# Kernel tuning notes

Hardware: AMD Instinct MI355X
Metric: run time of the kernel (lower is better)

The kernel has to match this reference:

```python
import jax, jax.numpy as jnp
import numpy as np

B = 1_048_576
NUM_USERS = 6041
NUM_MOVIES = 3953
EMB_DIM = 32
NUM_GENRES = 18
HIDDEN = [64, 32, 16]
WIDE_DIM = NUM_USERS + NUM_MOVIES + 3 + NUM_GENRES  # gender, age, occupation scalars
DEEP_IN = 2 * EMB_DIM + 3 + NUM_GENRES              # = 85


def setup_inputs() -> dict:
    key = jax.random.key(0)
    ks = jax.random.split(key, 20)
    inp = {
        "user_ids": jax.random.randint(ks[0], (B,), 0, NUM_USERS),
        "movie_ids": jax.random.randint(ks[1], (B,), 0, NUM_MOVIES),
        "gender": jax.random.uniform(ks[2], (B,), dtype=jnp.float32),
        "age": jax.random.uniform(ks[3], (B,), dtype=jnp.float32),
        "occupation": jax.random.uniform(ks[4], (B,), dtype=jnp.float32),
        "genres": jax.random.uniform(ks[5], (B, NUM_GENRES), dtype=jnp.float32),
        # wide linear (out_features=1): weight vector + scalar bias
        "wide_W": jax.random.normal(ks[6], (WIDE_DIM,), dtype=jnp.float32) * 0.01,
        "wide_b": jnp.zeros((), dtype=jnp.float32),
        # embedding tables
        "user_table": jax.random.normal(ks[7], (NUM_USERS, EMB_DIM), dtype=jnp.float32) * 0.05,
        "movie_table": jax.random.normal(ks[8], (NUM_MOVIES, EMB_DIM), dtype=jnp.float32) * 0.05,
        # deep MLP params (stored as [in, out])
        "W1": jax.random.normal(ks[9], (DEEP_IN, HIDDEN[0]), dtype=jnp.float32) * 0.05,
        "b1": jnp.zeros((HIDDEN[0],), dtype=jnp.float32),
        "W2": jax.random.normal(ks[10], (HIDDEN[0], HIDDEN[1]), dtype=jnp.float32) * 0.05,
        "b2": jnp.zeros((HIDDEN[1],), dtype=jnp.float32),
        "W3": jax.random.normal(ks[11], (HIDDEN[1], HIDDEN[2]), dtype=jnp.float32) * 0.05,
        "b3": jnp.zeros((HIDDEN[2],), dtype=jnp.float32),
        "W4": jax.random.normal(ks[12], (HIDDEN[2], 1), dtype=jnp.float32) * 0.05,
        "b4": jnp.zeros((1,), dtype=jnp.float32),
    }
    return inp


def reference(user_ids, movie_ids, gender, age, occupation, genres,
              wide_W, wide_b, user_table, movie_table,
              W1, b1, W2, b2, W3, b3, W4, b4):
    nu = user_table.shape[0]
    nm = movie_table.shape[0]
    # dense (non-one-hot) part of the wide input: [B, 3 + num_genres]
    rest = jnp.concatenate(
        [gender[:, None], age[:, None], occupation[:, None], genres], axis=1)
    # one_hot @ W  ==  gather of the corresponding weight entries (same math,
    # without materializing the [B, nu+nm+21] one-hot matrix)
    w_user = wide_W[:nu]
    w_movie = wide_W[nu:nu + nm]
    w_rest = wide_W[nu + nm:]
    wide_out = w_user[user_ids] + w_movie[movie_ids] + rest @ w_rest + wide_b  # [B]

    # deep path (dropout is identity at inference)
    u_emb = user_table[user_ids]    # [B, 32]
    m_emb = movie_table[movie_ids]  # [B, 32]
    h = jnp.concatenate([u_emb, m_emb, rest], axis=1)  # [B, 85]
    h = jax.nn.relu(h @ W1 + b1)
    h = jax.nn.relu(h @ W2 + b2)
    h = jax.nn.relu(h @ W3 + b3)
    deep_out = (h @ W4 + b4)[:, 0]  # [B]

    return jax.nn.sigmoid(wide_out + deep_out)  # [B]
```

## Files before the change

kernel.cpp:

```cpp
#include <hip/hip_runtime.h>

#define NUSERS  6041
#define NMOVIES 3953
#define EMB     32
#define NGEN    18
#define H1N     64
#define H2N     32
#define H3N     16

typedef __bf16 bf16_t;
typedef bf16_t bf16x8 __attribute__((ext_vector_type(8)));
typedef bf16_t bf16x4 __attribute__((ext_vector_type(4)));
typedef float  f32x4  __attribute__((ext_vector_type(4)));
typedef float  f32x8  __attribute__((ext_vector_type(8)));

__device__ __forceinline__ f32x4 mfma16(bf16x8 a, bf16x8 b, f32x4 c) {
    return __builtin_amdgcn_mfma_f32_16x16x32_bf16(a, b, c, 0, 0, 0);
}
__device__ __forceinline__ bf16x8 cvt8(f32x8 v) {
    bf16x8 o;
    #pragma unroll
    for (int i = 0; i < 8; ++i) o[i] = (bf16_t)v[i];
    return o;
}

#define L1STRIDE 68
#define L2STRIDE 36
#define RSTRIDE  28
#define RBUFSZ   (16 * RSTRIDE)

#define RESTW 24
#define PREPROWS 512

#define TAB_U4   (NUSERS * EMB / 4)
#define TAB_M4   (NMOVIES * EMB / 4)
#define TAB4TOT  (TAB_U4 + TAB_M4)

__device__ __forceinline__ void pack_rest_row(const float* __restrict__ x,
                                              float gg, float aa, float oo,
                                              bf16_t* __restrict__ op)
{
    bf16x8 c0, c1, c2;
    c0[0] = (bf16_t)gg;   c0[1] = (bf16_t)aa;   c0[2] = (bf16_t)oo;
    c0[3] = (bf16_t)x[0]; c0[4] = (bf16_t)x[1]; c0[5] = (bf16_t)x[2];
    c0[6] = (bf16_t)x[3]; c0[7] = (bf16_t)x[4];
    #pragma unroll
    for (int j = 0; j < 8; ++j) c1[j] = (bf16_t)x[5 + j];
    #pragma unroll
    for (int j = 0; j < 5; ++j) c2[j] = (bf16_t)x[13 + j];
    c2[5] = (bf16_t)0.0f;
    c2[6] = (bf16_t)1.0f;
    c2[7] = (bf16_t)0.0f;
    *(bf16x8*)(op)      = c0;
    *(bf16x8*)(op + 8)  = c1;
    *(bf16x8*)(op + 16) = c2;
}

__global__ __launch_bounds__(256)
void prep_all(const float* __restrict__ gender,
              const float* __restrict__ age,
              const float* __restrict__ occupation,
              const float* __restrict__ genres,
              const float* __restrict__ user_table,
              const float* __restrict__ movie_table,
              bf16_t* __restrict__ rest,
              bf16_t* __restrict__ utab,
              bf16_t* __restrict__ mtab,
              int n)
{
    const int t  = threadIdx.x;
    const int b  = blockIdx.x;
    const int gB = (n + PREPROWS - 1) / PREPROWS;

    if (b < gB) {
        const int r0 = b * PREPROWS;
        if ((n & 1) == 0) {
            __shared__ float gbuf[PREPROWS * NGEN];
            const float4* gsrc = (const float4*)genres;
            const int totF4  = (n * NGEN) >> 2;
            const int f4base = (r0 >> 1) * 9;
            #pragma unroll
            for (int s = 0; s < 9; ++s) {
                const int gi = t + s * 256;
                int idx = f4base + gi;
                if (idx > totF4 - 1) idx = totF4 - 1;
                *(float4*)(gbuf + gi * 4) = gsrc[idx];
            }
            __syncthreads();
            #pragma unroll
            for (int rr = 0; rr < 2; ++rr) {
                const int lr = t + rr * 256;
                const int r  = r0 + lr;
                if (r < n) {
                    float x[NGEN];
                    #pragma unroll
                    for (int c = 0; c < NGEN; ++c) x[c] = gbuf[lr * NGEN + c];
                    pack_rest_row(x, gender[r], age[r], occupation[r],
                                  rest + (size_t)r * RESTW);
                }
            }
        } else {
            for (int rr = 0; rr < 2; ++rr) {
                const int r = r0 + t + rr * 256;
                if (r < n) {
                    const float* gr = genres + (size_t)r * NGEN;
                    float x[NGEN];
                    #pragma unroll
                    for (int c = 0; c < NGEN; ++c) x[c] = gr[c];
                    pack_rest_row(x, gender[r], age[r], occupation[r],
                                  rest + (size_t)r * RESTW);
                }
            }
        }
    } else {
        const int u = (b - gB) * 256 + t;
        if (u < TAB4TOT) {
            if (u < TAB_U4) {
                float4 v = *(const float4*)(user_table + (size_t)u * 4);
                bf16x4 o; o[0]=(bf16_t)v.x; o[1]=(bf16_t)v.y; o[2]=(bf16_t)v.z; o[3]=(bf16_t)v.w;
                *(bf16x4*)(utab + (size_t)u * 4) = o;
            } else {
                const int w = u - TAB_U4;
                float4 v = *(const float4*)(movie_table + (size_t)w * 4);
                bf16x4 o; o[0]=(bf16_t)v.x; o[1]=(bf16_t)v.y; o[2]=(bf16_t)v.z; o[3]=(bf16_t)v.w;
                *(bf16x4*)(mtab + (size_t)w * 4) = o;
            }
        }
    }
}

__global__ __launch_bounds__(256, 2)
void wd_fwd_main(const int*   __restrict__ user_ids,
                 const int*   __restrict__ movie_ids,
                 const float* __restrict__ wide_W,
                 const float* __restrict__ wide_b,
                 const float* __restrict__ W1,
                 const float* __restrict__ b1,
                 const float* __restrict__ W2,
                 const float* __restrict__ b2,
                 const float* __restrict__ W3,
                 const float* __restrict__ b3,
                 const float* __restrict__ W4,
                 const float* __restrict__ b4,
                 const bf16_t* __restrict__ utab,
                 const bf16_t* __restrict__ mtab,
                 const bf16_t* __restrict__ rest,
                 float*       __restrict__ out,
                 int n)
{
    const int lane = threadIdx.x & 63;
    const int m    = lane & 15;
    const int quad = lane >> 4;

    bf16x8 B1f[3][4];
    #pragma unroll
    for (int kt = 0; kt < 3; ++kt)
        #pragma unroll
        for (int nt = 0; nt < 4; ++nt) {
            bf16x8 f;
            #pragma unroll
            for (int j = 0; j < 8; ++j) {
                const int k = kt * 32 + quad * 8 + j;
                float v;
                if (k < 85)       v = W1[k * H1N + nt * 16 + m];
                else if (k == 86) v = b1[nt * 16 + m];
                else              v = 0.0f;
                f[j] = (bf16_t)v;
            }
            B1f[kt][nt] = f;
        }
    bf16x8 Bwf;
    {
        const float* wr = wide_W + NUSERS + NMOVIES;
        #pragma unroll
        for (int j = 0; j < 8; ++j) {
            const int k = 64 + quad * 8 + j;
            float v = 0.0f;
            if (m == 0) { if (k < 85) v = wr[k - 64]; else if (k == 85) v = 1.0f; }
            Bwf[j] = (bf16_t)v;
        }
    }
    bf16x8 B2f[2][2];
    #pragma unroll
    for (int kt = 0; kt < 2; ++kt)
        #pragma unroll
        for (int nt = 0; nt < 2; ++nt) {
            bf16x8 f;
            #pragma unroll
            for (int j = 0; j < 8; ++j) {
                const int u = (2 * kt + (j >> 2)) * 16 + quad * 4 + (j & 3);
                f[j] = (bf16_t)W2[u * H2N + nt * 16 + m];
            }
            B2f[kt][nt] = f;
        }
    bf16x8 B3f;
    #pragma unroll
    for (int j = 0; j < 8; ++j) {
        const int u = (j >> 2) * 16 + quad * 4 + (j & 3);
        B3f[j] = (bf16_t)W3[u * H3N + m];
    }

    f32x4 bias2[2], bias3, w4f;
    bias2[0] = *(const f32x4*)(b2 + quad * 4);
    bias2[1] = *(const f32x4*)(b2 + 16 + quad * 4);
    bias3    = *(const f32x4*)(b3 + quad * 4);
    w4f      = *(const f32x4*)(W4 + quad * 4);
    const float b4v = b4[0];
    const float wb0 = wide_b[0];

    const int ntiles = (n + 15) >> 4;
    const int gwave  = (blockIdx.x * blockDim.x + threadIdx.x) >> 6;
    const int nwaves = (gridDim.x * blockDim.x) >> 6;
    int niter = 0;
    if (gwave < ntiles) niter = (ntiles - gwave + nwaves - 1) / nwaves;
    if (niter == 0) return;

    int t_c = gwave;
    int t_n = t_c + nwaves; if (t_n >= ntiles) t_n = t_c;

    int rc = t_c * 16 + m; if (rc >= n) rc = n - 1;
    int uid_c = user_ids[rc], mid_c = movie_ids[rc];
    bf16x8 A0c = *(const bf16x8*)(utab + (size_t)uid_c * EMB + quad * 8);
    bf16x8 A1c = *(const bf16x8*)(mtab + (size_t)mid_c * EMB + quad * 8);
    bf16x8 A2c;
    #pragma unroll
    for (int j = 0; j < 8; ++j) A2c[j] = (bf16_t)0.0f;
    if (quad < 3) A2c = *(const bf16x8*)(rest + (size_t)rc * RESTW + quad * 8);
    float wuc = 0.0f, wmc = 0.0f;
    if (quad == 2) { wuc = wide_W[uid_c]; wmc = wide_W[NUSERS + mid_c]; }
    int rn = t_n * 16 + m; if (rn >= n) rn = n - 1;
    int uid_n = user_ids[rn], mid_n = movie_ids[rn];

    for (int i = 0; i < niter; ++i) {
        const bool more = (i + 1 < niter);
        bf16x8 A0n = A0c, A1n = A1c, A2n;
        #pragma unroll
        for (int j = 0; j < 8; ++j) A2n[j] = (bf16_t)0.0f;
        float wun = wuc, wmn = wmc;
        int uid_n2 = uid_n, mid_n2 = mid_n;
        int t_n2 = t_n;
        if (more) {
            A0n = *(const bf16x8*)(utab + (size_t)uid_n * EMB + quad * 8);
            A1n = *(const bf16x8*)(mtab + (size_t)mid_n * EMB + quad * 8);
            int rx = t_n * 16 + m; if (rx >= n) rx = n - 1;
            if (quad < 3) A2n = *(const bf16x8*)(rest + (size_t)rx * RESTW + quad * 8);
            wun = 0.0f; wmn = 0.0f;
            if (quad == 2) { wun = wide_W[uid_n]; wmn = wide_W[NUSERS + mid_n]; }
            t_n2 = t_n + nwaves; if (t_n2 >= ntiles) t_n2 = t_n;
            int r2 = t_n2 * 16 + m; if (r2 >= n) r2 = n - 1;
            uid_n2 = user_ids[r2]; mid_n2 = movie_ids[r2];
        }

        bf16x8 A2 = A2c;
        if (quad == 2) A2[5] = (bf16_t)(wuc + wmc + wb0);

        f32x4 accw = mfma16(Bwf, A2, (f32x4){0.f, 0.f, 0.f, 0.f});

        f32x4 acc[4];
        #pragma unroll
        for (int nt = 0; nt < 4; ++nt) {
            f32x4 c = {0.f, 0.f, 0.f, 0.f};
            c = mfma16(B1f[2][nt], A2,  c);
            c = mfma16(B1f[1][nt], A1c, c);
            c = mfma16(B1f[0][nt], A0c, c);
            acc[nt] = c;
        }

        bf16x8 AL2[2];
        #pragma unroll
        for (int kt = 0; kt < 2; ++kt) {
            bf16x8 f;
            #pragma unroll
            for (int r = 0; r < 4; ++r) {
                f[r]     = (bf16_t)fmaxf(acc[2 * kt][r],     0.0f);
                f[4 + r] = (bf16_t)fmaxf(acc[2 * kt + 1][r], 0.0f);
            }
            AL2[kt] = f;
        }

        f32x4 acc2[2];
        #pragma unroll
        for (int nt = 0; nt < 2; ++nt) {
            f32x4 c = bias2[nt];
            c = mfma16(B2f[0][nt], AL2[0], c);
            c = mfma16(B2f[1][nt], AL2[1], c);
            acc2[nt] = c;
        }

        bf16x8 AL3;
        #pragma unroll
        for (int r = 0; r < 4; ++r) {
            AL3[r]     = (bf16_t)fmaxf(acc2[0][r], 0.0f);
            AL3[4 + r] = (bf16_t)fmaxf(acc2[1][r], 0.0f);
        }

        f32x4 acc3 = mfma16(B3f, AL3, bias3);

        float p = fmaxf(acc3[0], 0.0f) * w4f[0]
                + fmaxf(acc3[1], 0.0f) * w4f[1]
                + fmaxf(acc3[2], 0.0f) * w4f[2]
                + fmaxf(acc3[3], 0.0f) * w4f[3];
        p += __shfl_xor(p, 16, 64);
        p += __shfl_xor(p, 32, 64);
        if (lane < 16) {
            const int orow = (t_c << 4) + lane;
            if (orow < n) {
                const float zv = p + accw[0] + b4v;
                out[orow] = 1.0f / (1.0f + __expf(-zv));
            }
        }

        if (more) {
            A0c = A0n; A1c = A1n; A2c = A2n;
            wuc = wun; wmc = wmn;
            uid_n = uid_n2; mid_n = mid_n2;
            t_c = t_n; t_n = t_n2;
        }
    }
}

struct Pref {
    float4 u0, u1, m0, m1;
    float  wu, wm;
};

__global__ __launch_bounds__(256)
void wd_fwd_pipe(const int*   __restrict__ user_ids,
                 const int*   __restrict__ movie_ids,
                 const float* __restrict__ gender,
                 const float* __restrict__ age,
                 const float* __restrict__ occupation,
                 const float* __restrict__ genres,
                 const float* __restrict__ wide_W,
                 const float* __restrict__ wide_b,
                 const float* __restrict__ user_table,
                 const float* __restrict__ movie_table,
                 const float* __restrict__ W1,
                 const float* __restrict__ b1,
                 const float* __restrict__ W2,
                 const float* __restrict__ b2,
                 const float* __restrict__ W3,
                 const float* __restrict__ b3,
                 const float* __restrict__ W4,
                 const float* __restrict__ b4,
                 float*       __restrict__ out,
                 int n)
{
    const int lane = threadIdx.x & 63;
    const int wib  = threadIdx.x >> 6;
    const int m    = lane & 15;
    const int quad = lane >> 4;

    __shared__ float lds_rest[4][2 * RBUFSZ];
    __shared__ float lds1[4][16 * L1STRIDE];
    __shared__ float lds2[4][16 * L2STRIDE];
    float* __restrict__ rbase = lds_rest[wib];
    float* __restrict__ L1p   = lds1[wib];
    float* __restrict__ L2p   = lds2[wib];

    for (int k = lane; k < 2 * RBUFSZ; k += 64) rbase[k] = 0.0f;

    bf16x8 B1f[3][4];
    #pragma unroll
    for (int kt = 0; kt < 3; ++kt)
        #pragma unroll
        for (int nt = 0; nt < 4; ++nt) {
            bf16x8 f;
            #pragma unroll
            for (int j = 0; j < 8; ++j) {
                const int k  = kt * 32 + quad * 8 + j;
                const float v = (k < 85) ? W1[k * H1N + nt * 16 + m] : 0.0f;
                f[j] = (bf16_t)v;
            }
            B1f[kt][nt] = f;
        }
    bf16x8 Bwf;
    {
        const float* wr = wide_W + NUSERS + NMOVIES;
        #pragma unroll
        for (int j = 0; j < 8; ++j) {
            const int k = 64 + quad * 8 + j;
            float v = 0.0f;
            if (m == 0) { if (k < 85) v = wr[k - 64]; else if (k == 85) v = 1.0f; }
            Bwf[j] = (bf16_t)v;
        }
    }
    bf16x8 B2f[2][2];
    #pragma unroll
    for (int kt = 0; kt < 2; ++kt)
        #pragma unroll
        for (int nt = 0; nt < 2; ++nt) {
            bf16x8 f;
            #pragma unroll
            for (int j = 0; j < 8; ++j)
                f[j] = (bf16_t)W2[(kt * 32 + quad * 8 + j) * H2N + nt * 16 + m];
            B2f[kt][nt] = f;
        }
    bf16x8 B3f;
    #pragma unroll
    for (int j = 0; j < 8; ++j) B3f[j] = (bf16_t)W3[(quad * 8 + j) * H3N + m];

    float bias1[4], bias2[2];
    #pragma unroll
    for (int nt = 0; nt < 4; ++nt) bias1[nt] = b1[nt * 16 + m];
    #pragma unroll
    for (int nt = 0; nt < 2; ++nt) bias2[nt] = b2[nt * 16 + m];
    const float bias3 = b3[m];
    const float w4v   = W4[m];
    const float b4v   = b4[0];
    const float wb0   = wide_b[0];

    const int ntiles = (n + 15) >> 4;
    const int gwave  = blockIdx.x * 4 + wib;
    const int nwaves = gridDim.x * 4;
    int niter = 0;
    if (gwave < ntiles) niter = (ntiles - gwave + nwaves - 1) / nwaves;
    const long gmax = (long)n * NGEN - 1;

#define LOAD_IDS(tt, U, M) { int rr = (tt) * 16 + m; rr = rr < n ? rr : n - 1; \
                             U = user_ids[rr]; M = movie_ids[rr]; }
#define LOAD_GENRES(tt, G, SC) { \
    const long gb = (long)(tt) * (16 * NGEN); \
    _Pragma("unroll") \
    for (int r = 0; r < 4; ++r) { long idx = gb + lane + r * 64; \
        idx = idx < gmax ? idx : gmax; G[r] = genres[idx]; } \
    { long idx = gb + lane + 256; idx = idx < gmax ? idx : gmax; \
      G[4] = (lane < 32) ? genres[idx] : 0.0f; } \
    { int rr = (tt) * 16 + m; rr = rr < n ? rr : n - 1; \
      const float* sp = (quad == 0) ? gender : (quad == 1) ? age : occupation; \
      SC = (quad < 3) ? sp[rr] : 0.0f; } }
#define WRITE_RBUF(B, G, SC) { \
    float* rb_ = rbase + (B) * RBUFSZ; \
    _Pragma("unroll") \
    for (int r = 0; r < 4; ++r) { int gi = lane + r * 64; int rw = gi / NGEN; \
        int cl = gi - rw * NGEN; rb_[rw * RSTRIDE + 3 + cl] = G[r]; } \
    if (lane < 32) { int gi = lane + 256; int rw = gi / NGEN; int cl = gi - rw * NGEN; \
        rb_[rw * RSTRIDE + 3 + cl] = G[4]; } \
    if (quad < 3) rb_[m * RSTRIDE + quad] = SC; }
#define ISSUE_GATHER(UID, MID, P) { \
    const float4* up_ = (const float4*)(user_table + (size_t)(UID) * EMB + quad * 8); \
    P.u0 = up_[0]; P.u1 = up_[1]; \
    const float4* mp_ = (const float4*)(movie_table + (size_t)(MID) * EMB + quad * 8); \
    P.m0 = mp_[0]; P.m1 = mp_[1]; \
    P.wu = wide_W[UID]; P.wm = wide_W[NUSERS + (MID)]; }

    if (niter > 0) {
        int t_c = gwave;
        int t_n = t_c + nwaves; if (t_n >= ntiles) t_n = t_c;

        int uid_c, mid_c, uid_n, mid_n, uid_n2, mid_n2;
        float gg_c[5], sc_c, gg_n[5], sc_n;
        Pref P_c, P_n;

        LOAD_IDS(t_c, uid_c, mid_c);
        LOAD_GENRES(t_c, gg_c, sc_c);
        ISSUE_GATHER(uid_c, mid_c, P_c);
        LOAD_IDS(t_n, uid_n, mid_n);
        WRITE_RBUF(0, gg_c, sc_c);
        uid_n2 = uid_n; mid_n2 = mid_n;
        int buf = 0;

        for (int i = 0; i < niter; ++i) {
            const float* rb = rbase + buf * RBUFSZ;
            const float4* sA = (const float4*)(rb + m * RSTRIDE + quad * 8);
            float4 a2a = sA[0], a2b = sA[1];

            const bool more = (i + 1 < niter);
            int t_n2 = t_n;
            if (more) {
                LOAD_GENRES(t_n, gg_n, sc_n);
                ISSUE_GATHER(uid_n, mid_n, P_n);
                t_n2 = t_n + nwaves; if (t_n2 >= ntiles) t_n2 = t_n;
                LOAD_IDS(t_n2, uid_n2, mid_n2);
            }

            const int base = t_c << 4;
            f32x8 vf;
            vf[0]=P_c.u0.x; vf[1]=P_c.u0.y; vf[2]=P_c.u0.z; vf[3]=P_c.u0.w;
            vf[4]=P_c.u1.x; vf[5]=P_c.u1.y; vf[6]=P_c.u1.z; vf[7]=P_c.u1.w;
            bf16x8 A0 = cvt8(vf);
            vf[0]=P_c.m0.x; vf[1]=P_c.m0.y; vf[2]=P_c.m0.z; vf[3]=P_c.m0.w;
            vf[4]=P_c.m1.x; vf[5]=P_c.m1.y; vf[6]=P_c.m1.z; vf[7]=P_c.m1.w;
            bf16x8 A1 = cvt8(vf);
            vf[0]=a2a.x; vf[1]=a2a.y; vf[2]=a2a.z; vf[3]=a2a.w;
            vf[4]=a2b.x; vf[5]=a2b.y; vf[6]=a2b.z; vf[7]=a2b.w;
            if (quad == 2) vf[5] = P_c.wu + P_c.wm + wb0;
            bf16x8 A2 = cvt8(vf);

            f32x4 accw = mfma16(A2, Bwf, (f32x4){0.f, 0.f, 0.f, 0.f});

            f32x4 acc[4];
            #pragma unroll
            for (int nt = 0; nt < 4; ++nt) {
                f32x4 c = {bias1[nt], bias1[nt], bias1[nt], bias1[nt]};
                c = mfma16(A0, B1f[0][nt], c);
                c = mfma16(A1, B1f[1][nt], c);
                c = mfma16(A2, B1f[2][nt], c);
                acc[nt] = c;
            }
            #pragma unroll
            for (int nt = 0; nt < 4; ++nt)
                #pragma unroll
                for (int r = 0; r < 4; ++r)
                    L1p[(quad * 4 + r) * L1STRIDE + nt * 16 + m] = fmaxf(acc[nt][r], 0.0f);

            bf16x8 AL2[2];
            #pragma unroll
            for (int kt = 0; kt < 2; ++kt) {
                const float4* s = (const float4*)(L1p + m * L1STRIDE + kt * 32 + quad * 8);
                float4 a = s[0], b = s[1];
                f32x8 t8; t8[0]=a.x; t8[1]=a.y; t8[2]=a.z; t8[3]=a.w;
                t8[4]=b.x; t8[5]=b.y; t8[6]=b.z; t8[7]=b.w;
                AL2[kt] = cvt8(t8);
            }

            f32x4 acc2[2];
            #pragma unroll
            for (int nt = 0; nt < 2; ++nt) {
                f32x4 c = {bias2[nt], bias2[nt], bias2[nt], bias2[nt]};
                c = mfma16(AL2[0], B2f[0][nt], c);
                c = mfma16(AL2[1], B2f[1][nt], c);
                acc2[nt] = c;
            }
            #pragma unroll
            for (int nt = 0; nt < 2; ++nt)
                #pragma unroll
                for (int r = 0; r < 4; ++r)
                    L2p[(quad * 4 + r) * L2STRIDE + nt * 16 + m] = fmaxf(acc2[nt][r], 0.0f);

            bf16x8 AL3;
            {
                const float4* s = (const float4*)(L2p + m * L2STRIDE + quad * 8);
                float4 a = s[0], b = s[1];
                f32x8 t8; t8[0]=a.x; t8[1]=a.y; t8[2]=a.z; t8[3]=a.w;
                t8[4]=b.x; t8[5]=b.y; t8[6]=b.z; t8[7]=b.w;
                AL3 = cvt8(t8);
            }

            f32x4 acc3 = mfma16(AL3, B3f, (f32x4){bias3, bias3, bias3, bias3});

            float t0 = fmaxf(acc3[0], 0.0f) * w4v + accw[0];
            float t1 = fmaxf(acc3[1], 0.0f) * w4v + accw[1];
            float t2 = fmaxf(acc3[2], 0.0f) * w4v + accw[2];
            float t3 = fmaxf(acc3[3], 0.0f) * w4v + accw[3];
            #pragma unroll
            for (int off = 1; off < 16; off <<= 1) {
                t0 += __shfl_xor(t0, off, 64);
                t1 += __shfl_xor(t1, off, 64);
                t2 += __shfl_xor(t2, off, 64);
                t3 += __shfl_xor(t3, off, 64);
            }
            if (m < 4) {
                float zv = t0;
                zv = (m == 1) ? t1 : zv;
                zv = (m == 2) ? t2 : zv;
                zv = (m == 3) ? t3 : zv;
                zv += b4v;
                const int orow = base + quad * 4 + m;
                if (orow < n) out[orow] = 1.0f / (1.0f + __expf(-zv));
            }

            if (more) {
                WRITE_RBUF(buf ^ 1, gg_n, sc_n);
                P_c = P_n;
                uid_c = uid_n; mid_c = mid_n;
                uid_n = uid_n2; mid_n = mid_n2;
                t_c = t_n; t_n = t_n2;
                buf ^= 1;
            }
        }
    }
#undef LOAD_IDS
#undef LOAD_GENRES
#undef WRITE_RBUF
#undef ISSUE_GATHER
}

extern "C" void kernel_launch(void* const* d_in, const int* in_sizes, int n_in,
                              void* d_out, int out_size, void* d_ws, size_t ws_size,
                              hipStream_t stream)
{
    const int*   user_ids   = (const int*)  d_in[0];
    const int*   movie_ids  = (const int*)  d_in[1];
    const float* gender     = (const float*)d_in[2];
    const float* age        = (const float*)d_in[3];
    const float* occupation = (const float*)d_in[4];
    const float* genres     = (const float*)d_in[5];
    const float* wide_W     = (const float*)d_in[6];
    const float* wide_b     = (const float*)d_in[7];
    const float* user_table = (const float*)d_in[8];
    const float* movie_table= (const float*)d_in[9];
    const float* W1         = (const float*)d_in[10];
    const float* b1         = (const float*)d_in[11];
    const float* W2         = (const float*)d_in[12];
    const float* b2         = (const float*)d_in[13];
    const float* W3         = (const float*)d_in[14];
    const float* b3         = (const float*)d_in[15];
    const float* W4         = (const float*)d_in[16];
    const float* b4         = (const float*)d_in[17];
    float*       out        = (float*)d_out;

    const int n = in_sizes[0];

    const size_t utab_bytes = ((size_t)NUSERS  * EMB * 2 + 255) & ~(size_t)255;
    const size_t mtab_bytes = ((size_t)NMOVIES * EMB * 2 + 255) & ~(size_t)255;
    const size_t rest_bytes = (size_t)n * RESTW * 2;
    const size_t need = utab_bytes + mtab_bytes + rest_bytes;

    if (d_ws != nullptr && ws_size >= need) {
        bf16_t* utab = (bf16_t*)d_ws;
        bf16_t* mtab = (bf16_t*)((char*)d_ws + utab_bytes);
        bf16_t* rest = (bf16_t*)((char*)d_ws + utab_bytes + mtab_bytes);

        const int gB      = (n + PREPROWS - 1) / PREPROWS;
        const int tblocks = (TAB4TOT + 255) / 256;
        prep_all<<<gB + tblocks, 256, 0, stream>>>(gender, age, occupation, genres,
                                                   user_table, movie_table,
                                                   rest, utab, mtab, n);
        wd_fwd_main<<<1024, 256, 0, stream>>>(user_ids, movie_ids, wide_W, wide_b,
                                              W1, b1, W2, b2, W3, b3, W4, b4,
                                              utab, mtab, rest, out, n);
    } else {
        wd_fwd_pipe<<<1024, 256, 0, stream>>>(user_ids, movie_ids, gender, age, occupation,
                                              genres, wide_W, wide_b, user_table, movie_table,
                                              W1, b1, W2, b2, W3, b3, W4, b4, out, n);
    }
}
```

Baseline: 217.5 us.

## Prepack MLP weight fragments in prep kernel and launch single-wave main blocks

The prep kernel now also builds the bf16 MFMA B-fragments for W1/b1, the wide dense weights, W2 and W3 into a packed workspace buffer. Each main-kernel wave then loads its fragments with vector loads instead of gathering and converting them scalar by scalar. The main kernel switches from 1024 blocks of 256 threads to 8192 blocks of 64 threads, and the prep kernel handles 256 rows per block instead of 512. A uid_c/mid_c rotation is also added to the pipelined loop, which may be a correctness fix or a partial change.

```diff
diff --git a/kernel.cpp b/kernel.cpp
--- a/kernel.cpp
+++ b/kernel.cpp
@@ -29,90 +29,88 @@
 #define RSTRIDE  28
 #define RBUFSZ   (16 * RSTRIDE)
 
-#define RESTW 24
-#define PREPROWS 512
-
 #define TAB_U4   (NUSERS * EMB / 4)
 #define TAB_M4   (NMOVIES * EMB / 4)
 #define TAB4TOT  (TAB_U4 + TAB_M4)
-
-__device__ __forceinline__ void pack_rest_row(const float* __restrict__ x,
-                                              float gg, float aa, float oo,
-                                              bf16_t* __restrict__ op)
-{
-    bf16x8 c0, c1, c2;
-    c0[0] = (bf16_t)gg;   c0[1] = (bf16_t)aa;   c0[2] = (bf16_t)oo;
-    c0[3] = (bf16_t)x[0]; c0[4] = (bf16_t)x[1]; c0[5] = (bf16_t)x[2];
-    c0[6] = (bf16_t)x[3]; c0[7] = (bf16_t)x[4];
-    #pragma unroll
-    for (int j = 0; j < 8; ++j) c1[j] = (bf16_t)x[5 + j];
-    #pragma unroll
-    for (int j = 0; j < 5; ++j) c2[j] = (bf16_t)x[13 + j];
-    c2[5] = (bf16_t)0.0f;
-    c2[6] = (bf16_t)1.0f;
-    c2[7] = (bf16_t)0.0f;
-    *(bf16x8*)(op)      = c0;
-    *(bf16x8*)(op + 8)  = c1;
-    *(bf16x8*)(op + 16) = c2;
-}
+#define TABBLOCKS ((TAB4TOT + 255) / 256)
+
+#define RESTW 24
+
+#define WPACK_BYTES 18432
 
 __global__ __launch_bounds__(256)
-void prep_all(const float* __restrict__ gender,
-              const float* __restrict__ age,
-              const float* __restrict__ occupation,
-              const float* __restrict__ genres,
-              const float* __restrict__ user_table,
-              const float* __restrict__ movie_table,
-              bf16_t* __restrict__ rest,
-              bf16_t* __restrict__ utab,
-              bf16_t* __restrict__ mtab,
-              int n)
+void prep_all3(const float* __restrict__ gender,
+               const float* __restrict__ age,
+               const float* __restrict__ occupation,
+               const float* __restrict__ genres,
+               const float* __restrict__ user_table,
+               const float* __restrict__ movie_table,
+               const float* __restrict__ W1,
+               const float* __restrict__ b1,
+               const float* __restrict__ W2,
+               const float* __restrict__ W3,
+               const float* __restrict__ wide_W,
+               bf16_t* __restrict__ rest,
+               bf16_t* __restrict__ utab,
+               bf16_t* __restrict__ mtab,
+               bf16_t* __restrict__ wpack,
+               int n)
 {
     const int t  = threadIdx.x;
     const int b  = blockIdx.x;
-    const int gB = (n + PREPROWS - 1) / PREPROWS;
+    const int gB = (n + 255) >> 8;
 
     if (b < gB) {
-        const int r0 = b * PREPROWS;
+        const int r0 = b * 256;
+        __shared__ float gbuf[256 * NGEN];
         if ((n & 1) == 0) {
-            __shared__ float gbuf[PREPROWS * NGEN];
             const float4* gsrc = (const float4*)genres;
             const int totF4  = (n * NGEN) >> 2;
             const int f4base = (r0 >> 1) * 9;
             #pragma unroll
-            for (int s = 0; s < 9; ++s) {
+            for (int s = 0; s < 5; ++s) {
                 const int gi = t + s * 256;
-                int idx = f4base + gi;
-                if (idx > totF4 - 1) idx = totF4 - 1;
-                *(float4*)(gbuf + gi * 4) = gsrc[idx];
-            }
-            __syncthreads();
-            #pragma unroll
-            for (int rr = 0; rr < 2; ++rr) {
-                const int lr = t + rr * 256;
-                const int r  = r0 + lr;
-                if (r < n) {
-                    float x[NGEN];
-                    #pragma unroll
-                    for (int c = 0; c < NGEN; ++c) x[c] = gbuf[lr * NGEN + c];
-                    pack_rest_row(x, gender[r], age[r], occupation[r],
-                                  rest + (size_t)r * RESTW);
+                if (gi < 1152) {
+                    int idx = f4base + gi;
+                    if (idx > totF4 - 1) idx = totF4 - 1;
+                    *(float4*)(gbuf + gi * 4) = gsrc[idx];
                 }
             }
         } else {
-            for (int rr = 0; rr < 2; ++rr) {
-                const int r = r0 + t + rr * 256;
-                if (r < n) {
-                    const float* gr = genres + (size_t)r * NGEN;
-                    float x[NGEN];
-                    #pragma unroll
-                    for (int c = 0; c < NGEN; ++c) x[c] = gr[c];
-                    pack_rest_row(x, gender[r], age[r], occupation[r],
-                                  rest + (size_t)r * RESTW);
-                }
-            }
-        }
-    } else {
+            for (int gi = t; gi < 256 * NGEN; gi += 256) {
+                long idx = (long)r0 * NGEN + gi;
+                long mx  = (long)n * NGEN - 1;
+                if (idx > mx) idx = mx;
+                gbuf[gi] = genres[idx];
+            }
+        }
+        __syncthreads();
+        const int r = r0 + t;
+        if (r < n) {
+            float x[NGEN];
+            #pragma unroll
+            for (int c = 0; c < NGEN; ++c) x[c] = gbuf[t * NGEN + c];
+            const float gg = gender[r], aa = age[r], oo = occupation[r];
+            bf16x8 c0, c1, c2;
+            c0[0] = (bf16_t)gg;   c0[1] = (bf16_t)aa;   c0[2] = (bf16_t)oo;
+            c0[3] = (bf16_t)x[0]; c0[4] = (bf16_t)x[1]; c0[5] = (bf16_t)x[2];
+            c0[6] = (bf16_t)x[3]; c0[7] = (bf16_t)x[4];
+            #pragma unroll
+            for (int j = 0; j < 8; ++j) c1[j] = (bf16_t)x[5 + j];
+            #pragma unroll
+            for (int j = 0; j < 5; ++j) c2[j] = (bf16_t)x[13 + j];
+            c2[5] = (bf16_t)0.0f;
+            c2[6] = (bf16_t)1.0f;
+            c2[7] = (bf16_t)0.0f;
+            bf16_t* op = rest + (size_t)r * RESTW;
+            *(bf16x8*)(op)      = c0;
+            *(bf16x8*)(op + 8)  = c1;
+            *(bf16x8*)(op + 16) = c2;
+        }
+        return;
+    }
+
+    if (b < gB + TABBLOCKS) {
         const int u = (b - gB) * 256 + t;
         if (u < TAB4TOT) {
             if (u < TAB_U4) {
@@ -126,79 +124,87 @@
                 *(bf16x4*)(mtab + (size_t)w * 4) = o;
             }
         }
+        return;
+    }
+
+    const int l  = t & 63;
+    const int f0 = t >> 6;
+    const int m  = l & 15;
+    const int q  = l >> 4;
+    const float* wr = wide_W + NUSERS + NMOVIES;
+
+    #pragma unroll
+    for (int p = 0; p < 5; ++p) {
+        const int f = f0 + p * 4;
+        if (f >= 18) break;
+        bf16x8 frag;
+        #pragma unroll
+        for (int j = 0; j < 8; ++j) {
+            float v = 0.0f;
+            if (f < 12) {
+                const int kt = f >> 2, nt = f & 3;
+                if (kt < 2) {
+                    v = W1[(kt * 32 + q * 8 + j) * H1N + nt * 16 + m];
+                } else if (q < 3) {
+                    const int idx = q * 8 + j;
+                    if (idx <= 20)      v = W1[(64 + idx) * H1N + nt * 16 + m];
+                    else if (idx == 22) v = b1[nt * 16 + m];
+                }
+            } else if (f == 12) {
+                if (m == 0 && q < 3) {
+                    const int idx = q * 8 + j;
+                    if (idx <= 20)      v = wr[idx];
+                    else if (idx == 21) v = 1.0f;
+                }
+            } else if (f < 17) {
+                const int kt = (f - 13) >> 1, nt = (f - 13) & 1;
+                const int u = (2 * kt + (j >> 2)) * 16 + q * 4 + (j & 3);
+                v = W2[u * H2N + nt * 16 + m];
+            } else {
+                const int u = (j >> 2) * 16 + q * 4 + (j & 3);
+                v = W3[u * H3N + m];
+            }
+            frag[j] = (bf16_t)v;
+        }
+        *(bf16x8*)(wpack + ((size_t)f * 64 + l) * 8) = frag;
     }
 }
 
-__global__ __launch_bounds__(256, 2)
-void wd_fwd_main(const int*   __restrict__ user_ids,
-                 const int*   __restrict__ movie_ids,
-                 const float* __restrict__ wide_W,
-                 const float* __restrict__ wide_b,
-                 const float* __restrict__ W1,
-                 const float* __restrict__ b1,
-                 const float* __restrict__ W2,
-                 const float* __restrict__ b2,
-                 const float* __restrict__ W3,
-                 const float* __restrict__ b3,
-                 const float* __restrict__ W4,
-                 const float* __restrict__ b4,
-                 const bf16_t* __restrict__ utab,
-                 const bf16_t* __restrict__ mtab,
-                 const bf16_t* __restrict__ rest,
-                 float*       __restrict__ out,
-                 int n)
+__global__ __launch_bounds__(64, 4)
+void wd_fwd_main4(const int*   __restrict__ user_ids,
+                  const int*   __restrict__ movie_ids,
+                  const float* __restrict__ wide_W,
+                  const float* __restrict__ wide_b,
+                  const float* __restrict__ b2,
+                  const float* __restrict__ b3,
+                  const float* __restrict__ W4,
+                  const float* __restrict__ b4,
+                  const bf16_t* __restrict__ utab,
+                  const bf16_t* __restrict__ mtab,
+                  const bf16_t* __restrict__ rest,
+                  const bf16_t* __restrict__ wpack,
+                  float*       __restrict__ out,
+                  int n)
 {
     const int lane = threadIdx.x & 63;
     const int m    = lane & 15;
     const int quad = lane >> 4;
 
+    const bf16x8* wp = (const bf16x8*)wpack;
     bf16x8 B1f[3][4];
     #pragma unroll
     for (int kt = 0; kt < 3; ++kt)
         #pragma unroll
-        for (int nt = 0; nt < 4; ++nt) {
-            bf16x8 f;
-            #pragma unroll
-            for (int j = 0; j < 8; ++j) {
-                const int k = kt * 32 + quad * 8 + j;
-                float v;
-                if (k < 85)       v = W1[k * H1N + nt * 16 + m];
-                else if (k == 86) v = b1[nt * 16 + m];
-                else              v = 0.0f;
-                f[j] = (bf16_t)v;
-            }
-            B1f[kt][nt] = f;
-        }
-    bf16x8 Bwf;
-    {
-        const float* wr = wide_W + NUSERS + NMOVIES;
-        #pragma unroll
-        for (int j = 0; j < 8; ++j) {
-            const int k = 64 + quad * 8 + j;
-            float v = 0.0f;
-            if (m == 0) { if (k < 85) v = wr[k - 64]; else if (k == 85) v = 1.0f; }
-            Bwf[j] = (bf16_t)v;
-        }
-    }
+        for (int nt = 0; nt < 4; ++nt)
+            B1f[kt][nt] = wp[(kt * 4 + nt) * 64 + lane];
+    const bf16x8 Bwf = wp[12 * 64 + lane];
     bf16x8 B2f[2][2];
     #pragma unroll
     for (int kt = 0; kt < 2; ++kt)
         #pragma unroll
-        for (int nt = 0; nt < 2; ++nt) {
-            bf16x8 f;
-            #pragma unroll
-            for (int j = 0; j < 8; ++j) {
-                const int u = (2 * kt + (j >> 2)) * 16 + quad * 4 + (j & 3);
-                f[j] = (bf16_t)W2[u * H2N + nt * 16 + m];
-            }
-            B2f[kt][nt] = f;
-        }
-    bf16x8 B3f;
-    #pragma unroll
-    for (int j = 0; j < 8; ++j) {
-        const int u = (j >> 2) * 16 + quad * 4 + (j & 3);
-        B3f[j] = (bf16_t)W3[u * H3N + m];
-    }
+        for (int nt = 0; nt < 2; ++nt)
+            B2f[kt][nt] = wp[(13 + kt * 2 + nt) * 64 + lane];
+    const bf16x8 B3f = wp[17 * 64 + lane];
 
     f32x4 bias2[2], bias3, w4f;
     bias2[0] = *(const f32x4*)(b2 + quad * 4);
@@ -313,6 +319,7 @@
         if (more) {
             A0c = A0n; A1c = A1n; A2c = A2n;
             wuc = wun; wmc = wmn;
+            uid_c = uid_n; mid_c = mid_n;
             uid_n = uid_n2; mid_n = mid_n2;
             t_c = t_n; t_n = t_n2;
         }
@@ -602,24 +609,26 @@
 
     const int n = in_sizes[0];
 
-    const size_t utab_bytes = ((size_t)NUSERS  * EMB * 2 + 255) & ~(size_t)255;
-    const size_t mtab_bytes = ((size_t)NMOVIES * EMB * 2 + 255) & ~(size_t)255;
-    const size_t rest_bytes = (size_t)n * RESTW * 2;
-    const size_t need = utab_bytes + mtab_bytes + rest_bytes;
+    const size_t utab_bytes  = ((size_t)NUSERS  * EMB * 2 + 255) & ~(size_t)255;
+    const size_t mtab_bytes  = ((size_t)NMOVIES * EMB * 2 + 255) & ~(size_t)255;
+    const size_t wpack_bytes = (WPACK_BYTES + 255) & ~(size_t)255;
+    const size_t rest_bytes  = (size_t)n * RESTW * 2;
+    const size_t need = utab_bytes + mtab_bytes + wpack_bytes + rest_bytes;
 
     if (d_ws != nullptr && ws_size >= need) {
-        bf16_t* utab = (bf16_t*)d_ws;
-        bf16_t* mtab = (bf16_t*)((char*)d_ws + utab_bytes);
-        bf16_t* rest = (bf16_t*)((char*)d_ws + utab_bytes + mtab_bytes);
-
-        const int gB      = (n + PREPROWS - 1) / PREPROWS;
-        const int tblocks = (TAB4TOT + 255) / 256;
-        prep_all<<<gB + tblocks, 256, 0, stream>>>(gender, age, occupation, genres,
-                                                   user_table, movie_table,
-                                                   rest, utab, mtab, n);
-        wd_fwd_main<<<1024, 256, 0, stream>>>(user_ids, movie_ids, wide_W, wide_b,
-                                              W1, b1, W2, b2, W3, b3, W4, b4,
-                                              utab, mtab, rest, out, n);
+        bf16_t* utab  = (bf16_t*)d_ws;
+        bf16_t* mtab  = (bf16_t*)((char*)d_ws + utab_bytes);
+        bf16_t* wpack = (bf16_t*)((char*)d_ws + utab_bytes + mtab_bytes);
+        bf16_t* rest  = (bf16_t*)((char*)d_ws + utab_bytes + mtab_bytes + wpack_bytes);
+
+        const int gB = (n + 255) >> 8;
+        prep_all3<<<gB + TABBLOCKS + 1, 256, 0, stream>>>(gender, age, occupation,
+                                                          genres, user_table, movie_table,
+                                                          W1, b1, W2, W3, wide_W,
+                                                          rest, utab, mtab, wpack, n);
+        wd_fwd_main4<<<8192, 64, 0, stream>>>(user_ids, movie_ids,
+                                              wide_W, wide_b, b2, b3, W4, b4,
+                                              utab, mtab, rest, wpack, out, n);
     } else {
         wd_fwd_pipe<<<1024, 256, 0, stream>>>(user_ids, movie_ids, gender, age, occupation,
                                               genres, wide_W, wide_b, user_table, movie_table,
```

After: 279.6 us. 1.29x slower.
